# Kernel optimization log

Hardware: AMD Instinct MI355X
Metric: run time of the kernel (lower is better)

Reference implementation:

```python
import jax, jax.numpy as jnp
import numpy as np

RNN = 512
ENC = 512
HID = 512
ATT_SIZE = 196
B = 1024


def setup_inputs() -> dict:
    key = jax.random.key(0)
    ks = jax.random.split(key, 20)
    s = 0.02
    d = {
        "h": jax.random.normal(ks[0], (B, RNN), jnp.float32),
        "sentinel": jax.random.normal(ks[1], (B, RNN), jnp.float32),
        "att_feats": jax.random.normal(ks[2], (B, ATT_SIZE, RNN), jnp.float32),
        "W_ctx2att": jax.random.normal(ks[3], (RNN, HID), jnp.float32) * s,
        "b_ctx2att": jnp.zeros((HID,), jnp.float32),
        "W_sl": jax.random.normal(ks[4], (RNN, ENC), jnp.float32) * s,
        "b_sl": jnp.zeros((ENC,), jnp.float32),
        "W_se": jax.random.normal(ks[5], (ENC, HID), jnp.float32) * s,
        "b_se": jnp.zeros((HID,), jnp.float32),
        "W_hl": jax.random.normal(ks[6], (RNN, ENC), jnp.float32) * s,
        "b_hl": jnp.zeros((ENC,), jnp.float32),
        "W_he": jax.random.normal(ks[7], (ENC, HID), jnp.float32) * s,
        "b_he": jnp.zeros((HID,), jnp.float32),
        "W_alpha": jax.random.normal(ks[8], (HID, 1), jnp.float32) * s,
        "b_alpha": jnp.zeros((1,), jnp.float32),
        "W_att2h": jax.random.normal(ks[9], (RNN, RNN), jnp.float32) * s,
        "b_att2h": jnp.zeros((RNN,), jnp.float32),
    }
    return d


def reference(h, sentinel, att_feats, W_ctx2att, b_ctx2att, W_sl, b_sl,
              W_se, b_se, W_hl, b_hl, W_he, b_he, W_alpha, b_alpha,
              W_att2h, b_att2h):
    # Eval mode: dropout is identity.
    # Project attention features: [B, 196, HID]
    p_att = jnp.einsum("bsd,dh->bsh", att_feats, W_ctx2att) + b_ctx2att
    # Sentinel branch
    sent_lin = jax.nn.relu(sentinel @ W_sl + b_sl)          # [B, ENC]
    sent_emb = sent_lin @ W_se + b_se                       # [B, HID]
    # Hidden-state branch
    h_lin = jnp.tanh(h @ W_hl + b_hl)                       # [B, ENC]
    h_emb = h_lin @ W_he + b_he                             # [B, HID]
    # Concat sentinel with visual features: [B, 197, *]
    img_all = jnp.concatenate([sent_lin[:, None, :], att_feats], axis=1)
    img_all_embed = jnp.concatenate([sent_emb[:, None, :], p_att], axis=1)
    # Additive attention scores over 197 positions
    hA = jnp.tanh(img_all_embed + h_emb[:, None, :])        # [B, 197, HID]
    scores = (jnp.einsum("bsh,ho->bso", hA, W_alpha) + b_alpha)[..., 0]  # [B, 197]
    alpha = jax.nn.softmax(scores, axis=-1)
    # Weighted context
    cHat = jnp.einsum("bs,bsd->bd", alpha, img_all)          # [B, RNN]
    atten_out = cHat + h_lin
    out = jnp.tanh(atten_out @ W_att2h + b_att2h)            # [B, RNN]
    return out
```

## Files before the change

### kernel.cpp

```cpp
#include <hip/hip_runtime.h>
#include <hip/hip_bf16.h>

#define KDIM 512
#define NDIM 512
#define ATT  196
#define NB   1024

typedef __attribute__((ext_vector_type(8))) short bf16x8;
typedef __attribute__((ext_vector_type(8))) unsigned short ushort8;
typedef __attribute__((ext_vector_type(4))) float f32x4;

typedef const __attribute__((address_space(1))) unsigned int gas_uint;
typedef __attribute__((address_space(3))) unsigned int las_uint;

__device__ __forceinline__ void gload16(const void* g, void* l) {
    __builtin_amdgcn_global_load_lds((gas_uint*)g, (las_uint*)l, 16, 0, 0);
}

__device__ __forceinline__ float fast_tanh(float x) {
    x = fminf(15.f, fmaxf(-15.f, x));
    float t = __expf(2.f * x);
    return (t - 1.f) / (t + 1.f);
}

__device__ __forceinline__ unsigned short f2bf(float x) {
    union { float f; unsigned u; } v; v.f = x;
    unsigned r = v.u + 0x7FFF + ((v.u >> 16) & 1);
    return (unsigned short)(r >> 16);
}

__device__ __forceinline__ unsigned pk2(float a, float b) {
    __hip_bfloat162 h = __float22bfloat162_rn(float2{a, b});
    union { __hip_bfloat162 h2; unsigned u; } c; c.h2 = h;
    return c.u;
}

__global__ __launch_bounds__(256) void prep_weights(
        const float* __restrict__ W0, const float* __restrict__ W1,
        const float* __restrict__ W2, const float* __restrict__ W3,
        const float* __restrict__ W4, const float* __restrict__ W5,
        unsigned short* __restrict__ Wt) {
    int w = blockIdx.x >> 6;
    int t = blockIdx.x & 63;
    int k0 = (t >> 3) << 6, n0 = (t & 7) << 6;
    const float* W = (w == 0) ? W0 : (w == 1) ? W1 : (w == 2) ? W2 :
                     (w == 3) ? W3 : (w == 4) ? W4 : W5;
    __shared__ float tile[64][65];
    int tid = threadIdx.x;
    int nc = tid & 15, kr = tid >> 4;
#pragma unroll
    for (int i = 0; i < 4; ++i) {
        int k = kr + i * 16;
        float4 v = *(const float4*)&W[(size_t)(k0 + k) * NDIM + n0 + nc * 4];
        tile[k][nc * 4 + 0] = v.x; tile[k][nc * 4 + 1] = v.y;
        tile[k][nc * 4 + 2] = v.z; tile[k][nc * 4 + 3] = v.w;
    }
    __syncthreads();
    int n = tid >> 2, ks = tid & 3;
    ushort8 v0, v1;
#pragma unroll
    for (int j = 0; j < 8; ++j) v0[j] = f2bf(tile[ks * 16 + j][n]);
#pragma unroll
    for (int j = 0; j < 8; ++j) v1[j] = f2bf(tile[ks * 16 + 8 + j][n]);
    size_t base = ((size_t)w << 18) + (size_t)(n0 + n) * KDIM + k0 + ks * 16;
    *(ushort8*)&Wt[base] = v0;
    *(ushort8*)&Wt[base + 8] = v1;
}

__global__ __launch_bounds__(256) void gemm64(
        const float* __restrict__ A0, const unsigned short* __restrict__ W0,
        const float* __restrict__ bia0, float* __restrict__ O0, int act0,
        const float* __restrict__ A1, const unsigned short* __restrict__ W1,
        const float* __restrict__ bia1, float* __restrict__ O1, int act1) {
    const int op = blockIdx.y;
    const float* A = op ? A1 : A0;
    const unsigned short* Bt = op ? W1 : W0;
    const float* bias = op ? bia1 : bia0;
    float* out = op ? O1 : O0;
    const int act = op ? act1 : act0;

    __shared__ unsigned short A_lds[2][64 * 32];
    __shared__ unsigned short B_lds[2][128 * 32];

    const int tid = threadIdx.x;
    const int gm0 = (blockIdx.x >> 2) * 64, gn0 = (blockIdx.x & 3) * 128;
    const int wid = tid >> 6, lane = tid & 63;
    const int wm = wid >> 1, wn = wid & 1;
    const int lr = lane & 15, lk = lane >> 4;

    const int arow = tid >> 2, akc = tid & 3;
    const float* aptr = A + (size_t)(gm0 + arow) * KDIM + akc * 8;
    const int aoff = arow * 32 + ((akc ^ ((arow >> 1) & 3)) << 3);

    auto stageB = [&](int kt, int buf) {
#pragma unroll
        for (int j = 0; j < 2; ++j) {
            int c = tid + j * 256;
            int col = c >> 2, slot = c & 3;
            const unsigned short* src = Bt + (size_t)(gn0 + col) * KDIM +
                                        ((slot ^ ((col >> 1) & 3)) << 3) + kt * 32;
            gload16(src, &B_lds[buf][c * 8]);
        }
    };

    f32x4 acc[2][4] = {};

    {
        float4 x0 = *(const float4*)aptr;
        float4 x1 = *(const float4*)(aptr + 4);
        stageB(0, 0);
        uint4 p;
        p.x = pk2(x0.x, x0.y); p.y = pk2(x0.z, x0.w);
        p.z = pk2(x1.x, x1.y); p.w = pk2(x1.z, x1.w);
        *(uint4*)&A_lds[0][aoff] = p;
    }
    __syncthreads();

    const int swk = ((lk ^ ((lr >> 1) & 3)) << 3);
    for (int kt = 0; kt < 16; ++kt) {
        const int buf = kt & 1;
        float4 x0, x1;
        if (kt < 15) {
            const float* ap = aptr + (kt + 1) * 32;
            x0 = *(const float4*)ap;
            x1 = *(const float4*)(ap + 4);
            stageB(kt + 1, buf ^ 1);
        }
        bf16x8 af[2], bfr[4];
#pragma unroll
        for (int m = 0; m < 2; ++m)
            af[m] = *(const bf16x8*)&A_lds[buf][(wm * 32 + m * 16 + lr) * 32 + swk];
#pragma unroll
        for (int n = 0; n < 4; ++n)
            bfr[n] = *(const bf16x8*)&B_lds[buf][(wn * 64 + n * 16 + lr) * 32 + swk];
#pragma unroll
        for (int m = 0; m < 2; ++m)
#pragma unroll
            for (int n = 0; n < 4; ++n)
                acc[m][n] = __builtin_amdgcn_mfma_f32_16x16x32_bf16(af[m], bfr[n], acc[m][n], 0, 0, 0);
        if (kt < 15) {
            uint4 p;
            p.x = pk2(x0.x, x0.y); p.y = pk2(x0.z, x0.w);
            p.z = pk2(x1.x, x1.y); p.w = pk2(x1.z, x1.w);
            *(uint4*)&A_lds[buf ^ 1][aoff] = p;
        }
        __syncthreads();
    }

#pragma unroll
    for (int m = 0; m < 2; ++m)
#pragma unroll
        for (int n = 0; n < 4; ++n) {
            int col = gn0 + wn * 64 + n * 16 + lr;
            float bsv = bias[col];
#pragma unroll
            for (int r = 0; r < 4; ++r) {
                int row = gm0 + wm * 32 + m * 16 + lk * 4 + r;
                float v = acc[m][n][r] + bsv;
                if (act == 0) v = fmaxf(v, 0.f);
                else if (act == 1) v = fast_tanh(v);
                out[(size_t)row * NDIM + col] = v;
            }
        }
}

__launch_bounds__(512, 4)
__global__ void gemm_score(const float* __restrict__ A,
                           const unsigned short* __restrict__ Bt,
                           const float* __restrict__ b_ctx,
                           const float* __restrict__ h_emb,
                           const float* __restrict__ Walpha,
                           float* __restrict__ score) {
    __shared__ char smem[81920];
    float (*A_f)[256 * 32] = (float (*)[256 * 32])smem;
    unsigned short (*B_lds)[128 * 32] = (unsigned short (*)[128 * 32])(smem + 65536);
    float* ch_s = (float*)smem;
    float* wa_s = (float*)(smem + 1536);
    float* s_red = (float*)(smem + 2048);

    const int tid  = threadIdx.x;
    const int bidx = blockIdx.x;
    const int xcd  = bidx & 7, u = bidx >> 3;
    const int mblk = xcd * 98 + (u >> 2), nblk = u & 3;
    const int gm0  = mblk * 256, gn0 = nblk * 128;

    const int wid = tid >> 6, lane = tid & 63;
    const int wm  = wid >> 1, wn = wid & 1;
    const int lr  = lane & 15, lk = lane >> 4;

    const float* asrc[4];
#pragma unroll
    for (int i = 0; i < 4; ++i) {
        int c = tid + i * 512;
        int row = c >> 3, g = c & 7;
        asrc[i] = A + (size_t)(gm0 + row) * KDIM + ((g ^ (row & 7)) << 2);
    }
    auto stageA = [&](int kt, int buf) {
#pragma unroll
        for (int i = 0; i < 4; ++i)
            gload16(asrc[i] + kt * 32, &A_f[buf][(tid + i * 512) * 4]);
    };

    const int bcol = tid >> 2, bslot = tid & 3;
    const unsigned short* bsrc = Bt + (size_t)(gn0 + bcol) * KDIM +
                                 ((bslot ^ ((bcol >> 1) & 3)) << 3);
    auto stageB = [&](int kt, int buf) {
        gload16(bsrc + kt * 32, &B_lds[buf][tid * 8]);
    };

    f32x4 acc[4][4] = {};
    const int swk = ((lk ^ ((lr >> 1) & 3)) << 3);
    const int arw = lr & 7;
    const int as0 = (lk * 2) ^ arw;
    const int as1 = (lk * 2 + 1) ^ arw;

    stageA(0, 0);
    stageB(0, 0);
    __syncthreads();

#pragma unroll 1
    for (int kt = 0; kt < 16; ++kt) {
        const int buf = kt & 1;
        if (kt < 15) {
            stageA(kt + 1, buf ^ 1);
            stageB(kt + 1, buf ^ 1);
        }
        bf16x8 af[4], bfr[4];
#pragma unroll
        for (int n = 0; n < 4; ++n)
            bfr[n] = *(const bf16x8*)&B_lds[buf][(wn * 64 + n * 16 + lr) * 32 + swk];
#pragma unroll
        for (int m = 0; m < 4; ++m) {
            const int rbase = (wm * 64 + m * 16 + lr) * 32;
            float4 fa = *(const float4*)&A_f[buf][rbase + as0 * 4];
            float4 fb = *(const float4*)&A_f[buf][rbase + as1 * 4];
            uint4 p;
            p.x = pk2(fa.x, fa.y); p.y = pk2(fa.z, fa.w);
            p.z = pk2(fb.x, fb.y); p.w = pk2(fb.z, fb.w);
            union { uint4 u; bf16x8 v; } cc; cc.u = p;
            af[m] = cc.v;
        }
#pragma unroll
        for (int m = 0; m < 4; ++m)
#pragma unroll
            for (int n = 0; n < 4; ++n)
                acc[m][n] = __builtin_amdgcn_mfma_f32_16x16x32_bf16(af[m], bfr[n], acc[m][n], 0, 0, 0);
        __syncthreads();
    }

    const int bb0 = gm0 / ATT;
    {
        int j = tid >> 7;
        int c = tid & 127;
        if (j < 3) {
            int bb = bb0 + j; if (bb > NB - 1) bb = NB - 1;
            ch_s[j * 128 + c] = b_ctx[gn0 + c] + h_emb[(size_t)bb * NDIM + gn0 + c];
        }
        if (tid < 128) wa_s[tid] = Walpha[gn0 + tid];
    }
    __syncthreads();

#pragma unroll
    for (int m = 0; m < 4; ++m) {
#pragma unroll
        for (int r = 0; r < 4; ++r) {
            int rloc = wm * 64 + m * 16 + lk * 4 + r;
            int rg = gm0 + rloc;
            int sel = rg / ATT - bb0;
            float sum = 0.f;
#pragma unroll
            for (int n = 0; n < 4; ++n) {
                int cloc = wn * 64 + n * 16 + lr;
                sum += fast_tanh(acc[m][n][r] + ch_s[sel * 128 + cloc]) * wa_s[cloc];
            }
            sum += __shfl_xor(sum, 1);
            sum += __shfl_xor(sum, 2);
            sum += __shfl_xor(sum, 4);
            sum += __shfl_xor(sum, 8);
            if (lr == 0) s_red[wn * 256 + rloc] = sum;
        }
    }
    __syncthreads();
    if (tid < 256) {
        float tot = s_red[tid] + s_red[256 + tid];
        int rg = gm0 + tid;
        int bb = rg / ATT;
        atomicAdd(&score[(size_t)bb * 197 + (rg - bb * ATT) + 1], tot);
    }
}

__global__ __launch_bounds__(256) void softmax_chat(
        const float* __restrict__ score, const float* __restrict__ sent_emb,
        const float* __restrict__ h_emb, const float* __restrict__ Walpha,
        const float* __restrict__ sent_lin, const float* __restrict__ h_lin,
        const float* __restrict__ att, float* __restrict__ atten_out) {
    int b = blockIdx.x, tid = threadIdx.x;
    __shared__ float al[200];
    __shared__ float r4[4];

    float2 se = ((const float2*)(sent_emb + (size_t)b * NDIM))[tid];
    float2 he = ((const float2*)(h_emb + (size_t)b * NDIM))[tid];
    float2 wa = ((const float2*)Walpha)[tid];
    float val = fast_tanh(se.x + he.x) * wa.x + fast_tanh(se.y + he.y) * wa.y;
#pragma unroll
    for (int o = 32; o; o >>= 1) val += __shfl_xor(val, o);
    if ((tid & 63) == 0) r4[tid >> 6] = val;
    __syncthreads();
    float ssent = r4[0] + r4[1] + r4[2] + r4[3];
    __syncthreads();

    float v = -1e30f;
    if (tid < 197) v = (tid == 0) ? ssent : score[(size_t)b * 197 + tid];
    float m = v;
#pragma unroll
    for (int o = 32; o; o >>= 1) m = fmaxf(m, __shfl_xor(m, o));
    if ((tid & 63) == 0) r4[tid >> 6] = m;
    __syncthreads();
    m = fmaxf(fmaxf(r4[0], r4[1]), fmaxf(r4[2], r4[3]));
    __syncthreads();
    float e = (tid < 197) ? __expf(v - m) : 0.f;
    float s = e;
#pragma unroll
    for (int o = 32; o; o >>= 1) s += __shfl_xor(s, o);
    if ((tid & 63) == 0) r4[tid >> 6] = s;
    __syncthreads();
    s = r4[0] + r4[1] + r4[2] + r4[3];
    if (tid < 197) al[tid] = e / s;
    __syncthreads();

    const float2* af = (const float2*)(att + (size_t)b * ATT * KDIM);
    float2 a0 = ((const float2*)(sent_lin + (size_t)b * KDIM))[tid];
    float w0 = al[0];
    float2 accv; accv.x = w0 * a0.x; accv.y = w0 * a0.y;
#pragma unroll 14
    for (int ss = 0; ss < ATT; ++ss) {
        float w = al[ss + 1];
        float2 x = af[(size_t)ss * 256 + tid];
        accv.x += w * x.x; accv.y += w * x.y;
    }
    float2 hl = ((const float2*)(h_lin + (size_t)b * KDIM))[tid];
    accv.x += hl.x; accv.y += hl.y;
    ((float2*)(atten_out + (size_t)b * KDIM))[tid] = accv;
}

extern "C" void kernel_launch(void* const* d_in, const int* in_sizes, int n_in,
                              void* d_out, int out_size, void* d_ws, size_t ws_size,
                              hipStream_t stream) {
    const float* h     = (const float*)d_in[0];
    const float* sent  = (const float*)d_in[1];
    const float* att   = (const float*)d_in[2];
    const float* W_ctx = (const float*)d_in[3];
    const float* b_ctx = (const float*)d_in[4];
    const float* W_sl  = (const float*)d_in[5];
    const float* b_sl  = (const float*)d_in[6];
    const float* W_se  = (const float*)d_in[7];
    const float* b_se  = (const float*)d_in[8];
    const float* W_hl  = (const float*)d_in[9];
    const float* b_hl  = (const float*)d_in[10];
    const float* W_he  = (const float*)d_in[11];
    const float* b_he  = (const float*)d_in[12];
    const float* W_al  = (const float*)d_in[13];
    const float* W_a2h = (const float*)d_in[15];
    const float* b_a2h = (const float*)d_in[16];
    float* out = (float*)d_out;

    char* ws = (char*)d_ws;
    unsigned short* Wt = (unsigned short*)ws;
    float* sent_lin = (float*)(ws + 6u * 512 * 1024);
    float* h_lin    = sent_lin + (size_t)NB * 512;
    float* h_emb    = h_lin    + (size_t)NB * 512;
    float* sent_emb = h_emb    + (size_t)NB * 512;
    float* scorebuf = sent_emb + (size_t)NB * 512;
    float* atten    = scorebuf + (size_t)NB * 197;

    const size_t WSZ = 512 * 512;
    prep_weights<<<384, 256, 0, stream>>>(W_sl, W_hl, W_he, W_ctx, W_a2h, W_se, Wt);
    hipMemsetAsync(scorebuf, 0, (size_t)NB * 197 * sizeof(float), stream);

    gemm64<<<dim3(64, 2), 256, 0, stream>>>(
        sent, Wt + 0 * WSZ, b_sl, sent_lin, 0,
        h,    Wt + 1 * WSZ, b_hl, h_lin,    1);
    gemm64<<<dim3(64, 2), 256, 0, stream>>>(
        h_lin,    Wt + 2 * WSZ, b_he, h_emb,    2,
        sent_lin, Wt + 5 * WSZ, b_se, sent_emb, 2);

    gemm_score<<<3136, 512, 0, stream>>>(att, Wt + 3 * WSZ, b_ctx, h_emb, W_al, scorebuf);

    softmax_chat<<<NB, 256, 0, stream>>>(scorebuf, sent_emb, h_emb, W_al,
                                         sent_lin, h_lin, att, atten);

    gemm64<<<dim3(64, 1), 256, 0, stream>>>(
        atten, Wt + 4 * WSZ, b_a2h, out, 1,
        atten, Wt + 4 * WSZ, b_a2h, out, 1);
}
```

Measured before the change: 370.1 us.

## Emit bf16 copy of att_feats from GEMM for the context reduction

```diff
diff --git a/kernel.cpp b/kernel.cpp
--- a/kernel.cpp
+++ b/kernel.cpp
@@ -170,7 +170,8 @@
                            const float* __restrict__ b_ctx,
                            const float* __restrict__ h_emb,
                            const float* __restrict__ Walpha,
-                           float* __restrict__ score) {
+                           float* __restrict__ score,
+                           unsigned short* __restrict__ attbf) {
     __shared__ char smem[81920];
     float (*A_f)[256 * 32] = (float (*)[256 * 32])smem;
     unsigned short (*B_lds)[128 * 32] = (unsigned short (*)[128 * 32])(smem + 65536);
@@ -188,6 +189,8 @@
     const int wm  = wid >> 1, wn = wid & 1;
     const int lr  = lane & 15, lk = lane >> 4;
 
+    const bool wrbf = (attbf != nullptr) && (nblk == 0) && (wn == 0);
+
     const float* asrc[4];
 #pragma unroll
     for (int i = 0; i < 4; ++i) {
@@ -226,6 +229,7 @@
             stageB(kt + 1, buf ^ 1);
         }
         bf16x8 af[4], bfr[4];
+        uint4 pk[4];
 #pragma unroll
         for (int n = 0; n < 4; ++n)
             bfr[n] = *(const bf16x8*)&B_lds[buf][(wn * 64 + n * 16 + lr) * 32 + swk];
@@ -237,8 +241,20 @@
             uint4 p;
             p.x = pk2(fa.x, fa.y); p.y = pk2(fa.z, fa.w);
             p.z = pk2(fb.x, fb.y); p.w = pk2(fb.z, fb.w);
+            pk[m] = p;
             union { uint4 u; bf16x8 v; } cc; cc.u = p;
             af[m] = cc.v;
+        }
+        if (wrbf) {
+#pragma unroll
+            for (int m = 0; m < 4; ++m) {
+                size_t rg = (size_t)(gm0 + wm * 64 + m * 16 + lr);
+                unsigned* dst = (unsigned*)(attbf + rg * KDIM) + kt * 16 + lk * 4;
+                uint2 lo; lo.x = pk[m].x; lo.y = pk[m].y;
+                uint2 hi; hi.x = pk[m].z; hi.y = pk[m].w;
+                *(uint2*)(dst)     = lo;
+                *(uint2*)(dst + 2) = hi;
+            }
         }
 #pragma unroll
         for (int m = 0; m < 4; ++m)
@@ -289,11 +305,13 @@
     }
 }
 
+template<int BF>
 __global__ __launch_bounds__(256) void softmax_chat(
         const float* __restrict__ score, const float* __restrict__ sent_emb,
         const float* __restrict__ h_emb, const float* __restrict__ Walpha,
         const float* __restrict__ sent_lin, const float* __restrict__ h_lin,
-        const float* __restrict__ att, float* __restrict__ atten_out) {
+        const float* __restrict__ att, const unsigned short* __restrict__ attbf,
+        float* __restrict__ atten_out) {
     int b = blockIdx.x, tid = threadIdx.x;
     __shared__ float al[200];
     __shared__ float r4[4];
@@ -328,15 +346,27 @@
     if (tid < 197) al[tid] = e / s;
     __syncthreads();
 
-    const float2* af = (const float2*)(att + (size_t)b * ATT * KDIM);
     float2 a0 = ((const float2*)(sent_lin + (size_t)b * KDIM))[tid];
     float w0 = al[0];
     float2 accv; accv.x = w0 * a0.x; accv.y = w0 * a0.y;
+    if (BF) {
+        const unsigned* af = (const unsigned*)attbf + (size_t)b * ATT * 256 + tid;
 #pragma unroll 14
-    for (int ss = 0; ss < ATT; ++ss) {
-        float w = al[ss + 1];
-        float2 x = af[(size_t)ss * 256 + tid];
-        accv.x += w * x.x; accv.y += w * x.y;
+        for (int ss = 0; ss < ATT; ++ss) {
+            float w = al[ss + 1];
+            unsigned uu = af[(size_t)ss * 256];
+            union { unsigned u; float f; } lo, hi;
+            lo.u = uu << 16; hi.u = uu & 0xffff0000u;
+            accv.x += w * lo.f; accv.y += w * hi.f;
+        }
+    } else {
+        const float2* af = (const float2*)(att + (size_t)b * ATT * KDIM);
+#pragma unroll 14
+        for (int ss = 0; ss < ATT; ++ss) {
+            float w = al[ss + 1];
+            float2 x = af[(size_t)ss * 256 + tid];
+            accv.x += w * x.x; accv.y += w * x.y;
+        }
     }
     float2 hl = ((const float2*)(h_lin + (size_t)b * KDIM))[tid];
     accv.x += hl.x; accv.y += hl.y;
@@ -372,6 +402,13 @@
     float* sent_emb = h_emb    + (size_t)NB * 512;
     float* scorebuf = sent_emb + (size_t)NB * 512;
     float* atten    = scorebuf + (size_t)NB * 197;
+    char* endp = (char*)(atten + (size_t)NB * 512);
+    size_t used = (size_t)(endp - ws);
+    used = (used + 255) & ~(size_t)255;
+    size_t attbf_bytes = (size_t)NB * ATT * KDIM * sizeof(unsigned short);
+    unsigned short* attbf = nullptr;
+    if (ws_size >= used + attbf_bytes)
+        attbf = (unsigned short*)(ws + used);
 
     const size_t WSZ = 512 * 512;
     prep_weights<<<384, 256, 0, stream>>>(W_sl, W_hl, W_he, W_ctx, W_a2h, W_se, Wt);
@@ -384,10 +421,15 @@
         h_lin,    Wt + 2 * WSZ, b_he, h_emb,    2,
         sent_lin, Wt + 5 * WSZ, b_se, sent_emb, 2);
 
-    gemm_score<<<3136, 512, 0, stream>>>(att, Wt + 3 * WSZ, b_ctx, h_emb, W_al, scorebuf);
-
-    softmax_chat<<<NB, 256, 0, stream>>>(scorebuf, sent_emb, h_emb, W_al,
-                                         sent_lin, h_lin, att, atten);
+    gemm_score<<<3136, 512, 0, stream>>>(att, Wt + 3 * WSZ, b_ctx, h_emb, W_al,
+                                         scorebuf, attbf);
+
+    if (attbf)
+        softmax_chat<1><<<NB, 256, 0, stream>>>(scorebuf, sent_emb, h_emb, W_al,
+                                                sent_lin, h_lin, att, attbf, atten);
+    else
+        softmax_chat<0><<<NB, 256, 0, stream>>>(scorebuf, sent_emb, h_emb, W_al,
+                                                sent_lin, h_lin, att, attbf, atten);
 
     gemm64<<<dim3(64, 1), 256, 0, stream>>>(
         atten, Wt + 4 * WSZ, b_a2h, out, 1,
```

Result: slower. 381.4 us (+3.1%).
